# Kernel optimization log

Hardware: AMD Instinct MI355X
Metric: run time of the kernel (lower is better)

The kernel has to match this reference:

```python
import jax, jax.numpy as jnp
import numpy as np

B, N, F, E, K, R, H = 16, 2048, 2048, 128, 10, 2, 2


def setup_inputs() -> dict:
    key = jax.random.key(0)
    ks = jax.random.split(key, 11)
    s = 0.1  # keep embeddings close so the Gaussian kernel does not underflow
    rel = jax.random.normal(ks[0], (B, E), jnp.float32) * s
    arg1 = jax.random.normal(ks[1], (B, E), jnp.float32) * s
    arg2 = jax.random.normal(ks[2], (B, E), jnp.float32) * s
    fact_rel = jax.random.normal(ks[3], (B, F, E), jnp.float32) * s
    fact_arg1 = jax.random.normal(ks[4], (B, F, E), jnp.float32) * s
    fact_arg2 = jax.random.normal(ks[5], (B, F, E), jnp.float32) * s
    entity_embeddings = jax.random.normal(ks[6], (B, N, E), jnp.float32) * s
    hop_W = jax.random.normal(ks[7], (R, H, E, E), jnp.float32) / jnp.sqrt(jnp.float32(E))
    hop_b = jax.random.normal(ks[8], (R, H, E), jnp.float32) * 0.01
    nb_facts = jax.random.randint(ks[9], (B,), F // 2, F + 1, jnp.int32)
    nb_entities = jax.random.randint(ks[10], (B,), N // 2, N + 1, jnp.int32)
    return dict(rel=rel, arg1=arg1, arg2=arg2, fact_rel=fact_rel,
                fact_arg1=fact_arg1, fact_arg2=fact_arg2,
                entity_embeddings=entity_embeddings, hop_W=hop_W, hop_b=hop_b,
                nb_facts=nb_facts, nb_entities=nb_entities)


def reference(rel, arg1, arg2, fact_rel, fact_arg1, fact_arg2,
              entity_embeddings, hop_W, hop_b, nb_facts, nb_entities):
    # Gaussian kernel k(x,y) = exp(-||x-y||^2 / 2), batched: x [B,T,E], y [B,F,E] -> [B,T,F]
    def kern(x, y):
        d2 = (jnp.sum(x * x, -1)[:, :, None] + jnp.sum(y * y, -1)[:, None, :]
              - 2.0 * jnp.einsum('bte,bfe->btf', x, y))
        return jnp.exp(-0.5 * d2)

    fact_mask = (jnp.arange(F) < nb_facts[:, None])[:, None, :]            # [B,1,F]
    ent_mask = (jnp.arange(N) < nb_entities[:, None]).astype(rel.dtype)    # [B,N]

    # BatchNeuralKB.score: max over (valid) facts of product of kernels. [B,T,E]x3 -> [B,T]
    def model_score(r, a1, a2):
        s = kern(r, fact_rel) * kern(a1, fact_arg1) * kern(a2, fact_arg2)  # [B,T,F]
        return jnp.max(jnp.where(fact_mask, s, 0.0), axis=-1)

    # BatchNeuralKB.forward, (s,p,?) -> score per candidate object entity. [B,1,E] -> [B,N]
    def forward_sp(r, a1):
        kr = jnp.where(fact_mask, kern(r, fact_rel) * kern(a1, fact_arg1), 0.0)  # [B,1,F]
        kE = kern(entity_embeddings, fact_arg2)                                  # [B,N,F]
        return jnp.max(kr * kE, axis=-1) * ent_mask                              # [B,N]

    # (?,p,o) -> score per candidate subject entity
    def forward_po(r, a2):
        kr = jnp.where(fact_mask, kern(r, fact_rel) * kern(a2, fact_arg2), 0.0)
        kE = kern(entity_embeddings, fact_arg1)
        return jnp.max(kr * kE, axis=-1) * ent_mask

    # r_score(depth=1) = max(depth_r_score(0), depth_r_score(1))
    # depth_r_score(0) == model.score
    scores_0 = model_score(rel[:, None], arg1[:, None], arg2[:, None])[:, 0]  # [B]

    global_res = None
    for r_idx in range(R):
        is_rev = (r_idx % 2 == 1)
        # LinearReformulator: hop relations from rel
        h1 = rel @ hop_W[r_idx, 0] + hop_b[r_idx, 0]  # [B,E]
        h2 = rel @ hop_W[r_idx, 1] + hop_b[r_idx, 1]
        # hop 1: r_hop -> scores over all entities, then top-k beam
        if is_rev:
            sp = forward_po(h1[:, None], arg1[:, None])  # [B,N]
        else:
            sp = forward_sp(h1[:, None], arg1[:, None])
        z_scores, z_idx = jax.lax.top_k(sp, K)                                  # [B,K]
        z_emb = jnp.take_along_axis(entity_embeddings, z_idx[:, :, None], axis=1)  # [B,K,E]
        # final hop: r_score(depth=0) == model.score with branched args
        h2k = jnp.broadcast_to(h2[:, None, :], (B, K, E))
        a2k = jnp.broadcast_to(arg2[:, None, :], (B, K, E))
        if is_rev:
            s2 = model_score(h2k, a2k, z_emb)  # [B,K]
        else:
            s2 = model_score(h2k, z_emb, a2k)
        rule_scores = jnp.minimum(s2, z_scores)   # tnorm = 'min'
        rule_res = jnp.max(rule_scores, axis=1)   # max over branches [B]
        global_res = rule_res if global_res is None else jnp.maximum(global_res, rule_res)

    return jnp.maximum(scores_0, global_res)
```

## Files before the change

### kernel.cpp

```cpp
#include <hip/hip_runtime.h>
#include <math.h>

#define Bb 16
#define Nn 2048
#define Ff 2048
#define Ee 128
#define Kk 10
#define S2FC 8
#define S2F (Ff / S2FC)
#define FS 2

typedef __attribute__((ext_vector_type(8))) short short8;
typedef __attribute__((ext_vector_type(4))) float f32x4;

__device__ inline float wave_sum(float x) {
    for (int o = 32; o; o >>= 1) x += __shfl_down(x, o);
    return x;
}

__device__ inline void bsplit(float x, unsigned short& h, unsigned short& l) {
    unsigned int u = __float_as_uint(x);
    h = (unsigned short)(u >> 16);
    float hf = __uint_as_float(u & 0xFFFF0000u);
    l = (unsigned short)(__float_as_uint(x - hf) >> 16);
}

__device__ inline void atomic_fmax_pos(float* addr, float v) {
    atomicMax((unsigned int*)addr, __float_as_uint(v));
}

__global__ __launch_bounds__(256) void k_pfe(
    const float* __restrict__ rel, const float* __restrict__ arg1,
    const float* __restrict__ arg2, const float* __restrict__ frel,
    const float* __restrict__ fa1, const float* __restrict__ fa2,
    const float* __restrict__ ent, const float* __restrict__ hop_W,
    const float* __restrict__ hop_b, const int* __restrict__ nb_facts,
    unsigned short* __restrict__ B0, unsigned short* __restrict__ B1,
    float* __restrict__ ent_norm, float* __restrict__ c0, float* __restrict__ c1,
    float* __restrict__ s2b0, float* __restrict__ s2b1,
    float* __restrict__ sp0, float* __restrict__ sp1, float* __restrict__ out) {
    int bx = blockIdx.x;
    int tid = threadIdx.x;
    if (bx < 128) {
        int fcb = bx & 7, b = bx >> 3;
        int nbf = nb_facts[b];
        if (fcb * 256 >= nbf) {
            int f = fcb * 256 + tid;
            size_t o = (size_t)b * Ff + f;
            const float NI = -INFINITY;
            c0[o] = NI; c1[o] = NI; s2b0[o] = NI; s2b1[o] = NI;
            return;
        }
        __shared__ float q[7][Ee];
        __shared__ float bred[4];
        if (tid < 128) {
            q[0][tid] = rel[b * Ee + tid];
            q[1][tid] = arg1[b * Ee + tid];
            q[2][tid] = arg2[b * Ee + tid];
        }
        __syncthreads();
        {
            int e = tid & 127, hf = tid >> 7;
            const float* W0 = hop_W + (size_t)(hf * 2) * Ee * Ee;
            const float* W1 = W0 + (size_t)Ee * Ee;
            float a0 = hop_b[(hf * 2) * Ee + e];
            float a1 = hop_b[(hf * 2 + 1) * Ee + e];
            for (int qq = 0; qq < Ee; ++qq) {
                float rq = q[0][qq];
                a0 += rq * W0[qq * Ee + e];
                a1 += rq * W1[qq * Ee + e];
            }
            q[3 + hf][e] = a0;
            q[5 + hf][e] = a1;
        }
        __syncthreads();

        int f = fcb * 256 + tid;
        const float* pr = frel + ((size_t)b * Ff + f) * Ee;
        const float* p1 = fa1 + ((size_t)b * Ff + f) * Ee;
        const float* p2 = fa2 + ((size_t)b * Ff + f) * Ee;
        float d_rr = 0, d_a11 = 0, d_a22 = 0, d_h10 = 0, d_h11 = 0, d_h20 = 0, d_h21 = 0;
        float d_a12 = 0, d_a21 = 0, n1 = 0, n2 = 0;
#pragma unroll 8
        for (int e0 = 0; e0 < Ee; e0 += 4) {
            float4 vr4 = *(const float4*)(pr + e0);
            float4 v14 = *(const float4*)(p1 + e0);
            float4 v24 = *(const float4*)(p2 + e0);
            const float* vrp = (const float*)&vr4;
            const float* v1p = (const float*)&v14;
            const float* v2p = (const float*)&v24;
#pragma unroll
            for (int j = 0; j < 4; ++j) {
                int e = e0 + j;
                float fr = vrp[j], f1 = v1p[j], f2 = v2p[j];
                float t;
                t = q[0][e] - fr; d_rr  += t * t;
                t = q[1][e] - f1; d_a11 += t * t;
                t = q[2][e] - f2; d_a22 += t * t;
                t = q[3][e] - fr; d_h10 += t * t;
                t = q[4][e] - fr; d_h11 += t * t;
                t = q[5][e] - fr; d_h20 += t * t;
                t = q[6][e] - fr; d_h21 += t * t;
                t = q[1][e] - f2; d_a12 += t * t;
                t = q[2][e] - f1; d_a21 += t * t;
                n1 += f1 * f1; n2 += f2 * f2;
            }
        }
        bool valid = f < nbf;
        const float NI = -INFINITY;
        size_t o = (size_t)b * Ff + f;
        c0[o]   = valid ? (-0.5f * (d_h10 + d_a11 + n2)) : NI;
        c1[o]   = valid ? (-0.5f * (d_h11 + d_a12 + n1)) : NI;
        s2b0[o] = valid ? (-0.5f * (d_h20 + d_a22)) : NI;
        s2b1[o] = valid ? (-0.5f * (d_h21 + d_a21)) : NI;
        float lsc = valid ? (-0.5f * (d_rr + d_a11 + d_a22)) : NI;
        for (int m = 32; m; m >>= 1) lsc = fmaxf(lsc, __shfl_down(lsc, m));
        if ((tid & 63) == 0) bred[tid >> 6] = lsc;
        __syncthreads();
        if (tid == 0) {
            float m = fmaxf(fmaxf(bred[0], bred[1]), fmaxf(bred[2], bred[3]));
            atomic_fmax_pos(out + b, expf(m));
        }
    } else if (bx < 128 + 4096) {
        __shared__ uint4 tlds[16 * 33];
        int bxx = bx - 128;
        int y = bxx >> 11, bxi = bxx & 2047;
        int oct = tid & 15, fl = tid >> 4;
        int b = bxi >> 7, fbase = (bxi & 127) * 16;
        const float* src = (y == 0) ? fa2 : fa1;
        const float* s = src + ((size_t)b * Ff + fbase + fl) * Ee + oct * 8;
        float4 v0 = *(const float4*)s;
        float4 v1 = *(const float4*)(s + 4);
        float xs[8] = {v0.x, v0.y, v0.z, v0.w, v1.x, v1.y, v1.z, v1.w};
        unsigned short hi[8], lo[8];
#pragma unroll
        for (int j = 0; j < 8; ++j) bsplit(xs[j], hi[j], lo[j]);
        uint4 ph, pl;
        ph.x = (unsigned)hi[0] | ((unsigned)hi[1] << 16);
        ph.y = (unsigned)hi[2] | ((unsigned)hi[3] << 16);
        ph.z = (unsigned)hi[4] | ((unsigned)hi[5] << 16);
        ph.w = (unsigned)hi[6] | ((unsigned)hi[7] << 16);
        pl.x = (unsigned)lo[0] | ((unsigned)lo[1] << 16);
        pl.y = (unsigned)lo[2] | ((unsigned)lo[3] << 16);
        pl.z = (unsigned)lo[4] | ((unsigned)lo[5] << 16);
        pl.w = (unsigned)lo[6] | ((unsigned)lo[7] << 16);
        tlds[fl * 33 + oct * 2]     = ph;
        tlds[fl * 33 + oct * 2 + 1] = pl;
        __syncthreads();
        int octw = tid >> 4, u0 = tid & 15;
        unsigned short* obase = ((y == 0) ? B0 : B1) +
                                (((size_t)b * 16 + octw) * Ff + fbase) * 16;
        int f0 = u0 >> 1, p0 = u0 & 1;
        int f1 = f0 + 8;
        *(uint4*)(obase + (size_t)u0 * 8)        = tlds[f0 * 33 + octw * 2 + p0];
        *(uint4*)(obase + (size_t)(u0 + 16) * 8) = tlds[f1 * 33 + octw * 2 + p0];
    } else {
        int row  = (bx - (128 + 4096)) * 4 + (tid >> 6);
        int lane = tid & 63;
        const float* p = ent + (size_t)row * Ee;
        float a = p[lane], c = p[lane + 64];
        float s = wave_sum(a * a + c * c);
        if (lane == 0) {
            ent_norm[row] = s;
            sp0[row] = 0.0f;
            sp1[row] = 0.0f;
        }
    }
}

#define BMs 256

__global__ __launch_bounds__(512, 2) void k_spmax_mfma(
    const float* __restrict__ ent, const unsigned short* __restrict__ B0,
    const unsigned short* __restrict__ B1, const float* __restrict__ c0,
    const float* __restrict__ c1, const float* __restrict__ ent_norm,
    const int* __restrict__ nb_facts, const int* __restrict__ nb_entities,
    float* __restrict__ sp0, float* __restrict__ sp1) {
    int bid = blockIdx.x;
    int br = bid & 31, nblk = (bid >> 5) & 7, h = bid >> 8;
    int b = br >> 1, r = br & 1;
    const unsigned short* Bt = (r == 0) ? B0 : B1;
    const float* cb = ((r == 0) ? c0 : c1) + (size_t)b * Ff;
    float* sp = ((r == 0) ? sp0 : sp1) + (size_t)b * Nn;

    int tid = threadIdx.x;
    int ne = nb_entities[b];
    if (nblk * BMs >= ne) return;
    int nch = (nb_facts[b] + 63) >> 6;
    if (h >= nch) return;

    __shared__ unsigned short alds[4 * 4 * 4 * 64 * 8];

    int wave = tid >> 6, lane = tid & 63;
    int wm = wave >> 1, wn = wave & 1;
    int lane15 = lane & 15, quad = lane >> 4;

    short8 ah[4][4];
    {
        const float* abase = ent + ((size_t)b * Nn + (size_t)nblk * BMs + wm * 64) * Ee;
#pragma unroll
        for (int i = 0; i < 4; ++i)
#pragma unroll
            for (int ks = 0; ks < 4; ++ks) {
                const float* p = abase + (size_t)(i * 16 + lane15) * Ee + ks * 32 + quad * 8;
                float4 v0 = *(const float4*)p;
                float4 v1 = *(const float4*)(p + 4);
                float xs[8] = {v0.x, v0.y, v0.z, v0.w, v1.x, v1.y, v1.z, v1.w};
                short8 hi8, lo8;
#pragma unroll
                for (int j = 0; j < 8; ++j) {
                    unsigned short hh, ll;
                    bsplit(xs[j], hh, ll);
                    hi8[j] = (short)hh;
                    lo8[j] = (short)ll;
                }
                ah[i][ks] = hi8;
                if (wn == 0)
                    *(short8*)&alds[(((wm * 4 + i) * 4 + ks) * 64 + lane) * 8] = lo8;
            }
    }
    __syncthreads();

    const unsigned short* bbase =
        Bt + ((((size_t)b * 16 + quad) * Ff) + wn * 32 + lane15) * 16;

    short8 pbh0[4], pbl0[4], pbh1[4], pbl1[4];
#pragma unroll
    for (int ks = 0; ks < 4; ++ks) {
        const unsigned short* p0 = bbase + ((size_t)ks * 4 * Ff + h * 64) * 16;
        pbh0[ks] = *(const short8*)p0;
        pbl0[ks] = *(const short8*)(p0 + 8);
        pbh1[ks] = *(const short8*)(p0 + 256);
        pbl1[ks] = *(const short8*)(p0 + 264);
    }
    short8 bufA[4], bufB[4];
#pragma unroll
    for (int i = 0; i < 4; ++i)
        bufA[i] = *(short8*)&alds[(((wm * 4 + i) * 4 + 0) * 64 + lane) * 8];

    float mmax[4][4];
#pragma unroll
    for (int i = 0; i < 4; ++i)
#pragma unroll
        for (int rr = 0; rr < 4; ++rr) mmax[i][rr] = -INFINITY;

    for (int c = h; c < nch; c += FS) {
        int f0 = c * 64;
        float cj0 = cb[f0 + wn * 32 + lane15];
        float cj1 = cb[f0 + wn * 32 + 16 + lane15];
        f32x4 acc[4][2];
#pragma unroll
        for (int i = 0; i < 4; ++i) {
            acc[i][0] = (f32x4){cj0, cj0, cj0, cj0};
            acc[i][1] = (f32x4){cj1, cj1, cj1, cj1};
        }
        int fn = ((c + FS < nch) ? (c + FS) : h) * 64;

#pragma unroll
        for (int ks = 0; ks < 4; ++ks) {
            short8 bh0 = pbh0[ks], bl0 = pbl0[ks], bh1 = pbh1[ks], bl1 = pbl1[ks];
            const unsigned short* p0 = bbase + ((size_t)ks * 4 * Ff + fn) * 16;
            pbh0[ks] = *(const short8*)p0;
            pbl0[ks] = *(const short8*)(p0 + 8);
            pbh1[ks] = *(const short8*)(p0 + 256);
            pbl1[ks] = *(const short8*)(p0 + 264);
            short8* cur = (ks & 1) ? bufB : bufA;
            short8* nxt = (ks & 1) ? bufA : bufB;
            int nks = (ks + 1) & 3;
#pragma unroll
            for (int i = 0; i < 4; ++i)
                nxt[i] = *(short8*)&alds[(((wm * 4 + i) * 4 + nks) * 64 + lane) * 8];
#pragma unroll
            for (int i = 0; i < 4; ++i) {
                acc[i][0] = __builtin_amdgcn_mfma_f32_16x16x32_bf16(ah[i][ks], bh0, acc[i][0], 0, 0, 0);
                acc[i][0] = __builtin_amdgcn_mfma_f32_16x16x32_bf16(cur[i],    bh0, acc[i][0], 0, 0, 0);
                acc[i][0] = __builtin_amdgcn_mfma_f32_16x16x32_bf16(ah[i][ks], bl0, acc[i][0], 0, 0, 0);
                acc[i][1] = __builtin_amdgcn_mfma_f32_16x16x32_bf16(ah[i][ks], bh1, acc[i][1], 0, 0, 0);
                acc[i][1] = __builtin_amdgcn_mfma_f32_16x16x32_bf16(cur[i],    bh1, acc[i][1], 0, 0, 0);
                acc[i][1] = __builtin_amdgcn_mfma_f32_16x16x32_bf16(ah[i][ks], bl1, acc[i][1], 0, 0, 0);
            }
        }

#pragma unroll
        for (int j = 0; j < 2; ++j)
#pragma unroll
            for (int i = 0; i < 4; ++i)
#pragma unroll
                for (int rr = 0; rr < 4; ++rr)
                    mmax[i][rr] = fmaxf(mmax[i][rr], acc[i][j][rr]);
    }

    __syncthreads();
    float* red = (float*)alds;
#pragma unroll
    for (int i = 0; i < 4; ++i)
#pragma unroll
        for (int rr = 0; rr < 4; ++rr) {
            float v = mmax[i][rr];
#pragma unroll
            for (int m = 1; m < 16; m <<= 1) v = fmaxf(v, __shfl_xor(v, m));
            if (lane15 == 0) red[(wm * 64 + i * 16 + quad * 4 + rr) * 2 + wn] = v;
        }
    __syncthreads();
    if (tid < BMs) {
        float m = fmaxf(red[tid * 2], red[tid * 2 + 1]);
        int n = nblk * BMs + tid;
        if (n < ne)
            atomic_fmax_pos(&sp[n], expf(m - 0.5f * ent_norm[(size_t)b * Nn + n]));
    }
}

__global__ __launch_bounds__(256) void k_s2t(
    const float* __restrict__ ent, const float* __restrict__ fa1,
    const float* __restrict__ fa2, const float* __restrict__ s2b0,
    const float* __restrict__ s2b1, const float* __restrict__ sp0,
    const float* __restrict__ sp1, const int* __restrict__ nb_facts,
    float* __restrict__ out) {
    int fc = blockIdx.x, b = blockIdx.y, r = blockIdx.z;
    if (fc * S2F >= nb_facts[b]) return;
    const float* factX = (r == 0) ? fa1 : fa2;
    const float* s2b   = ((r == 0) ? s2b0 : s2b1) + (size_t)b * Ff;
    const float* sp    = ((r == 0) ? sp0 : sp1) + (size_t)b * Nn;

    __shared__ float zsc[Kk];
    __shared__ int   zidx[Kk];
    __shared__ float zsh[Kk][Ee];
    __shared__ float znorm[Kk];
    __shared__ float red[4][Kk];
    __shared__ float rules[Kk];

    int tid = threadIdx.x;
    int wv = tid >> 6, lane = tid & 63;

    if (wv == 0) {
        float v[Nn / 64];
#pragma unroll
        for (int i = 0; i < Nn / 64; ++i) v[i] = sp[i * 64 + lane];
        for (int k = 0; k < Kk; ++k) {
            float best = -INFINITY; int bidx = 0;
#pragma unroll
            for (int i = 0; i < Nn / 64; ++i)
                if (v[i] > best) { best = v[i]; bidx = i * 64 + lane; }
#pragma unroll
            for (int m = 1; m < 64; m <<= 1) {
                float ov = __shfl_xor(best, m);
                int oi = __shfl_xor(bidx, m);
                if (ov > best || (ov == best && oi < bidx)) { best = ov; bidx = oi; }
            }
            if (lane == 0) { zsc[k] = best; zidx[k] = bidx; }
            if ((bidx & 63) == lane) {
                int slot = bidx >> 6;
#pragma unroll
                for (int i = 0; i < Nn / 64; ++i)
                    if (i == slot) v[i] = -INFINITY;
            }
        }
    }
    __syncthreads();
    for (int idx = tid; idx < Kk * Ee; idx += 256) {
        int k = idx >> 7, e = idx & 127;
        zsh[k][e] = ent[((size_t)b * Nn + zidx[k]) * Ee + e];
    }
    __syncthreads();
    if (tid < Kk) {
        float s = 0.f;
        for (int e = 0; e < Ee; ++e) { float v = zsh[tid][e]; s += v * v; }
        znorm[tid] = s;
    }
    __syncthreads();

    int f = fc * S2F + tid;
    const float* fp = factX + ((size_t)b * Ff + f) * Ee;
    float acc[Kk];
#pragma unroll
    for (int k = 0; k < Kk; ++k) acc[k] = 0.f;
    float nf = 0.f;
#pragma unroll 4
    for (int e0 = 0; e0 < Ee; e0 += 4) {
        float4 v = *(const float4*)(fp + e0);
        nf += v.x * v.x + v.y * v.y + v.z * v.z + v.w * v.w;
#pragma unroll
        for (int k = 0; k < Kk; ++k) {
            float4 z = *(const float4*)&zsh[k][e0];
            acc[k] += z.x * v.x + z.y * v.y + z.z * v.z + z.w * v.w;
        }
    }
    float base = s2b[f] - 0.5f * nf;
    float sc[Kk];
#pragma unroll
    for (int k = 0; k < Kk; ++k) sc[k] = base + acc[k] - 0.5f * znorm[k];
    for (int o = 32; o; o >>= 1)
#pragma unroll
        for (int k = 0; k < Kk; ++k) sc[k] = fmaxf(sc[k], __shfl_down(sc[k], o));
    if ((tid & 63) == 0)
#pragma unroll
        for (int k = 0; k < Kk; ++k) red[wv][k] = sc[k];
    __syncthreads();
    if (tid < Kk) {
        float m = fmaxf(fmaxf(red[0][tid], red[1][tid]), fmaxf(red[2][tid], red[3][tid]));
        rules[tid] = fminf(expf(m), zsc[tid]);
    }
    __syncthreads();
    if (tid == 0) {
        float g = rules[0];
#pragma unroll
        for (int k = 1; k < Kk; ++k) g = fmaxf(g, rules[k]);
        atomic_fmax_pos(out + b, g);
    }
}

extern "C" void kernel_launch(void* const* d_in, const int* in_sizes, int n_in,
                              void* d_out, int out_size, void* d_ws, size_t ws_size,
                              hipStream_t stream) {
    const float* rel  = (const float*)d_in[0];
    const float* arg1 = (const float*)d_in[1];
    const float* arg2 = (const float*)d_in[2];
    const float* frel = (const float*)d_in[3];
    const float* fa1  = (const float*)d_in[4];
    const float* fa2  = (const float*)d_in[5];
    const float* ent  = (const float*)d_in[6];
    const float* hopW = (const float*)d_in[7];
    const float* hopb = (const float*)d_in[8];
    const int* nb_facts    = (const int*)d_in[9];
    const int* nb_entities = (const int*)d_in[10];
    float* out = (float*)d_out;

    float* ws = (float*)d_ws;
    size_t off = 0;
    float* c0       = ws + off; off += (size_t)Bb * Ff;
    float* c1       = ws + off; off += (size_t)Bb * Ff;
    float* s2b0     = ws + off; off += (size_t)Bb * Ff;
    float* s2b1     = ws + off; off += (size_t)Bb * Ff;
    float* sp0      = ws + off; off += (size_t)Bb * Nn;
    float* sp1      = ws + off; off += (size_t)Bb * Nn;
    float* ent_norm = ws + off; off += (size_t)Bb * Nn;
    off = (off + 7) & ~(size_t)7;
    unsigned short* B0 = (unsigned short*)(ws + off); off += (size_t)Bb * 16 * Ff * 8;
    unsigned short* B1 = (unsigned short*)(ws + off); off += (size_t)Bb * 16 * Ff * 8;

    hipMemsetAsync(d_out, 0, (size_t)out_size * sizeof(float), stream);
    k_pfe<<<dim3(128 + 4096 + Bb * Nn / 4), 256, 0, stream>>>(
        rel, arg1, arg2, frel, fa1, fa2, ent, hopW, hopb, nb_facts,
        B0, B1, ent_norm, c0, c1, s2b0, s2b1, sp0, sp1, out);
    k_spmax_mfma<<<dim3(32 * 8 * FS), 512, 0, stream>>>(ent, B0, B1, c0, c1, ent_norm,
                                                        nb_facts, nb_entities, sp0, sp1);
    k_s2t<<<dim3(S2FC, Bb, 2), 256, 0, stream>>>(ent, fa1, fa2, s2b0, s2b1,
                                                 sp0, sp1, nb_facts, out);
}
```

Before: 240.7 us.

## Stage B tiles into LDS via async global_load_lds double buffering, drop fact split

The B operand (bf16 hi/lo fact data) is now written in a swizzled chunk layout by the prep kernel and streamed into double-buffered LDS with global_load_lds, replacing per-lane register prefetch from global memory. The A low part now stays in registers instead of LDS. The fact-dimension split (FS=2) is removed, so one block covers all fact chunks and writes sp directly instead of using an atomic max. This halves the grid to 256 blocks, which costs parallelism and adds a barrier per chunk in exchange for shared, coalesced B loads.

```diff
diff --git a/kernel.cpp b/kernel.cpp
--- a/kernel.cpp
+++ b/kernel.cpp
@@ -8,10 +8,10 @@
 #define Kk 10
 #define S2FC 8
 #define S2F (Ff / S2FC)
-#define FS 2
 
 typedef __attribute__((ext_vector_type(8))) short short8;
 typedef __attribute__((ext_vector_type(4))) float f32x4;
+typedef unsigned int u32;
 
 __device__ inline float wave_sum(float x) {
     for (int o = 32; o; o >>= 1) x += __shfl_down(x, o);
@@ -28,6 +28,13 @@
 __device__ inline void atomic_fmax_pos(float* addr, float v) {
     atomicMax((unsigned int*)addr, __float_as_uint(v));
 }
+
+__device__ inline void gload_lds16(const void* g, void* l) {
+    __builtin_amdgcn_global_load_lds(
+        (const __attribute__((address_space(1))) u32*)g,
+        (__attribute__((address_space(3))) u32*)l, 16, 0, 0);
+}
+
 
 __global__ __launch_bounds__(256) void k_pfe(
     const float* __restrict__ rel, const float* __restrict__ arg1,
@@ -147,13 +154,20 @@
         tlds[fl * 33 + oct * 2]     = ph;
         tlds[fl * 33 + oct * 2 + 1] = pl;
         __syncthreads();
-        int octw = tid >> 4, u0 = tid & 15;
-        unsigned short* obase = ((y == 0) ? B0 : B1) +
-                                (((size_t)b * 16 + octw) * Ff + fbase) * 16;
-        int f0 = u0 >> 1, p0 = u0 & 1;
-        int f1 = f0 + 8;
-        *(uint4*)(obase + (size_t)u0 * 8)        = tlds[f0 * 33 + octw * 2 + p0];
-        *(uint4*)(obase + (size_t)(u0 + 16) * 8) = tlds[f1 * 33 + octw * 2 + p0];
+        int F4 = (fbase >> 4) & 1, F5 = (fbase >> 5) & 1;
+        unsigned char* ob = (unsigned char*)((y == 0) ? B0 : B1) +
+                            (((size_t)b << 20) + (size_t)(fbase >> 6) * 32768 +
+                             F5 * 1024 + F4 * 512);
+#pragma unroll
+        for (int uu = 0; uu < 2; ++uu) {
+            int u = tid + uu * 256;
+            int o = u >> 5, sS = u & 31;
+            int s0 = sS & 1, s1 = (sS >> 1) & 1, s2 = (sS >> 2) & 1;
+            int s3 = (sS >> 3) & 1, s4 = (sS >> 4) & 1;
+            int part = s0 ^ s3;
+            int fll = (s1 ^ s4) | ((s2 ^ F4) << 1) | (s3 << 2) | (s4 << 3);
+            *(uint4*)(ob + o * 2048 + sS * 16) = tlds[fll * 33 + o * 2 + part];
+        }
     } else {
         int row  = (bx - (128 + 4096)) * 4 + (tid >> 6);
         int lane = tid & 63;
@@ -177,7 +191,7 @@
     const int* __restrict__ nb_facts, const int* __restrict__ nb_entities,
     float* __restrict__ sp0, float* __restrict__ sp1) {
     int bid = blockIdx.x;
-    int br = bid & 31, nblk = (bid >> 5) & 7, h = bid >> 8;
+    int br = bid & 31, nblk = bid >> 5;
     int b = br >> 1, r = br & 1;
     const unsigned short* Bt = (r == 0) ? B0 : B1;
     const float* cb = ((r == 0) ? c0 : c1) + (size_t)b * Ff;
@@ -187,15 +201,14 @@
     int ne = nb_entities[b];
     if (nblk * BMs >= ne) return;
     int nch = (nb_facts[b] + 63) >> 6;
-    if (h >= nch) return;
-
-    __shared__ unsigned short alds[4 * 4 * 4 * 64 * 8];
+
+    __shared__ uint4 ldsB4[2 * 2048];
 
     int wave = tid >> 6, lane = tid & 63;
     int wm = wave >> 1, wn = wave & 1;
     int lane15 = lane & 15, quad = lane >> 4;
 
-    short8 ah[4][4];
+    short8 ah[4][4], al[4][4];
     {
         const float* abase = ent + ((size_t)b * Nn + (size_t)nblk * BMs + wm * 64) * Ee;
 #pragma unroll
@@ -215,68 +228,66 @@
                     lo8[j] = (short)ll;
                 }
                 ah[i][ks] = hi8;
-                if (wn == 0)
-                    *(short8*)&alds[(((wm * 4 + i) * 4 + ks) * 64 + lane) * 8] = lo8;
-            }
-    }
-    __syncthreads();
-
-    const unsigned short* bbase =
-        Bt + ((((size_t)b * 16 + quad) * Ff) + wn * 32 + lane15) * 16;
-
-    short8 pbh0[4], pbl0[4], pbh1[4], pbl1[4];
-#pragma unroll
-    for (int ks = 0; ks < 4; ++ks) {
-        const unsigned short* p0 = bbase + ((size_t)ks * 4 * Ff + h * 64) * 16;
-        pbh0[ks] = *(const short8*)p0;
-        pbl0[ks] = *(const short8*)(p0 + 8);
-        pbh1[ks] = *(const short8*)(p0 + 256);
-        pbl1[ks] = *(const short8*)(p0 + 264);
-    }
-    short8 bufA[4], bufB[4];
+                al[i][ks] = lo8;
+            }
+    }
+
+    int offA = (wn * 32 + lane15) * 32;
+    int physA0 = offA ^ (((offA >> 7) & 7) << 4);
+    int offB = offA + 512;
+    int physB0 = offB ^ (((offB >> 7) & 7) << 4);
+    int qoff = quad * 2048;
+
+    unsigned char* ldsB = (unsigned char*)ldsB4;
+    const unsigned char* gB = (const unsigned char*)Bt + ((size_t)b << 20);
+
+#pragma unroll
+    for (int t = 0; t < 4; ++t) {
+        int seg = t * 8 + wave;
+        gload_lds16(gB + seg * 1024 + lane * 16, ldsB + seg * 1024);
+    }
+    __syncthreads();
+
+    float mmax[4][4];
 #pragma unroll
     for (int i = 0; i < 4; ++i)
-        bufA[i] = *(short8*)&alds[(((wm * 4 + i) * 4 + 0) * 64 + lane) * 8];
-
-    float mmax[4][4];
-#pragma unroll
-    for (int i = 0; i < 4; ++i)
 #pragma unroll
         for (int rr = 0; rr < 4; ++rr) mmax[i][rr] = -INFINITY;
 
-    for (int c = h; c < nch; c += FS) {
-        int f0 = c * 64;
-        float cj0 = cb[f0 + wn * 32 + lane15];
-        float cj1 = cb[f0 + wn * 32 + 16 + lane15];
+    int cur = 0;
+    for (int c = 0; c < nch; ++c) {
+        if (c + 1 < nch) {
+            const unsigned char* gc = gB + (size_t)(c + 1) * 32768;
+            unsigned char* lb = ldsB + (cur ^ 1) * 32768;
+#pragma unroll
+            for (int t = 0; t < 4; ++t) {
+                int seg = t * 8 + wave;
+                gload_lds16(gc + seg * 1024 + lane * 16, lb + seg * 1024);
+            }
+        }
+        float cj0 = cb[c * 64 + wn * 32 + lane15];
+        float cj1 = cb[c * 64 + wn * 32 + 16 + lane15];
         f32x4 acc[4][2];
 #pragma unroll
         for (int i = 0; i < 4; ++i) {
             acc[i][0] = (f32x4){cj0, cj0, cj0, cj0};
             acc[i][1] = (f32x4){cj1, cj1, cj1, cj1};
         }
-        int fn = ((c + FS < nch) ? (c + FS) : h) * 64;
-
+        const unsigned char* bb = ldsB + cur * 32768;
 #pragma unroll
         for (int ks = 0; ks < 4; ++ks) {
-            short8 bh0 = pbh0[ks], bl0 = pbl0[ks], bh1 = pbh1[ks], bl1 = pbl1[ks];
-            const unsigned short* p0 = bbase + ((size_t)ks * 4 * Ff + fn) * 16;
-            pbh0[ks] = *(const short8*)p0;
-            pbl0[ks] = *(const short8*)(p0 + 8);
-            pbh1[ks] = *(const short8*)(p0 + 256);
-            pbl1[ks] = *(const short8*)(p0 + 264);
-            short8* cur = (ks & 1) ? bufB : bufA;
-            short8* nxt = (ks & 1) ? bufA : bufB;
-            int nks = (ks + 1) & 3;
-#pragma unroll
-            for (int i = 0; i < 4; ++i)
-                nxt[i] = *(short8*)&alds[(((wm * 4 + i) * 4 + nks) * 64 + lane) * 8];
+            const unsigned char* bk = bb + ks * 8192 + qoff;
+            short8 bh0 = *(const short8*)(bk + physA0);
+            short8 bl0 = *(const short8*)(bk + (physA0 ^ 16));
+            short8 bh1 = *(const short8*)(bk + physB0);
+            short8 bl1 = *(const short8*)(bk + (physB0 ^ 16));
 #pragma unroll
             for (int i = 0; i < 4; ++i) {
                 acc[i][0] = __builtin_amdgcn_mfma_f32_16x16x32_bf16(ah[i][ks], bh0, acc[i][0], 0, 0, 0);
-                acc[i][0] = __builtin_amdgcn_mfma_f32_16x16x32_bf16(cur[i],    bh0, acc[i][0], 0, 0, 0);
+                acc[i][0] = __builtin_amdgcn_mfma_f32_16x16x32_bf16(al[i][ks], bh0, acc[i][0], 0, 0, 0);
                 acc[i][0] = __builtin_amdgcn_mfma_f32_16x16x32_bf16(ah[i][ks], bl0, acc[i][0], 0, 0, 0);
                 acc[i][1] = __builtin_amdgcn_mfma_f32_16x16x32_bf16(ah[i][ks], bh1, acc[i][1], 0, 0, 0);
-                acc[i][1] = __builtin_amdgcn_mfma_f32_16x16x32_bf16(cur[i],    bh1, acc[i][1], 0, 0, 0);
+                acc[i][1] = __builtin_amdgcn_mfma_f32_16x16x32_bf16(al[i][ks], bh1, acc[i][1], 0, 0, 0);
                 acc[i][1] = __builtin_amdgcn_mfma_f32_16x16x32_bf16(ah[i][ks], bl1, acc[i][1], 0, 0, 0);
             }
         }
@@ -288,10 +299,12 @@
 #pragma unroll
                 for (int rr = 0; rr < 4; ++rr)
                     mmax[i][rr] = fmaxf(mmax[i][rr], acc[i][j][rr]);
-    }
-
-    __syncthreads();
-    float* red = (float*)alds;
+
+        __syncthreads();
+        cur ^= 1;
+    }
+
+    float* red = (float*)ldsB;
 #pragma unroll
     for (int i = 0; i < 4; ++i)
 #pragma unroll
@@ -306,7 +319,7 @@
         float m = fmaxf(red[tid * 2], red[tid * 2 + 1]);
         int n = nblk * BMs + tid;
         if (n < ne)
-            atomic_fmax_pos(&sp[n], expf(m - 0.5f * ent_norm[(size_t)b * Nn + n]));
+            sp[n] = expf(m - 0.5f * ent_norm[(size_t)b * Nn + n]);
     }
 }
 
@@ -442,8 +455,8 @@
     k_pfe<<<dim3(128 + 4096 + Bb * Nn / 4), 256, 0, stream>>>(
         rel, arg1, arg2, frel, fa1, fa2, ent, hopW, hopb, nb_facts,
         B0, B1, ent_norm, c0, c1, s2b0, s2b1, sp0, sp1, out);
-    k_spmax_mfma<<<dim3(32 * 8 * FS), 512, 0, stream>>>(ent, B0, B1, c0, c1, ent_norm,
-                                                        nb_facts, nb_entities, sp0, sp1);
+    k_spmax_mfma<<<dim3(32 * 8), 512, 0, stream>>>(ent, B0, B1, c0, c1, ent_norm,
+                                                   nb_facts, nb_entities, sp0, sp1);
     k_s2t<<<dim3(S2FC, Bb, 2), 256, 0, stream>>>(ent, fa1, fa2, s2b0, s2b1,
                                                  sp0, sp1, nb_facts, out);
 }
```

After: 225.5 us (median of 2 runs). -6.3%, faster.
